# Performance work log

Measured on AMD Instinct MI355X. Metric: run time of the kernel, lower is better.

## Reference

```python
import itertools
import jax, jax.numpy as jnp
import numpy as np

B, S, D = 512, 49, 448
H, KD, RATIO, RES = 8, 32, 4, 7
EKD = KD * RATIO              # expanded key dim = 128
QKV_OUT = H * (2 * KD + EKD)  # 1536
MLP_HID = D * 4               # 1792
EPS = 1e-5
LS_INIT = 1e-5


def _build_bias_idxs():
    points = list(itertools.product(range(RES), range(RES)))
    offsets = {}
    idxs = []
    for p1 in points:
        for p2 in points:
            off = (abs(p1[0] - p2[0]), abs(p1[1] - p2[1]))
            if off not in offsets:
                offsets[off] = len(offsets)
            idxs.append(offsets[off])
    return np.asarray(idxs, dtype=np.int32).reshape(len(points), len(points)), len(offsets)


def setup_inputs() -> dict:
    key = jax.random.key(0)
    ks = jax.random.split(key, 10)
    idxs_np, n_off = _build_bias_idxs()  # (49,49), 49 unique offsets
    std = 0.02
    return {
        "hidden_states": jax.random.normal(ks[0], (B, S, D), jnp.float32),
        "ln1_g": jnp.ones((D,), jnp.float32),
        "ln1_b": jnp.zeros((D,), jnp.float32),
        "qkv_w": jax.random.normal(ks[1], (D, QKV_OUT), jnp.float32) * std,
        "qkv_b": jnp.zeros((QKV_OUT,), jnp.float32),
        "attention_biases": jax.random.normal(ks[2], (H, n_off), jnp.float32) * std,
        "proj_w": jax.random.normal(ks[3], (H * EKD, D), jnp.float32) * std,
        "proj_b": jnp.zeros((D,), jnp.float32),
        "ln2_g": jnp.ones((D,), jnp.float32),
        "ln2_b": jnp.zeros((D,), jnp.float32),
        "mlp_w1": jax.random.normal(ks[4], (D, MLP_HID), jnp.float32) * std,
        "mlp_b1": jnp.zeros((MLP_HID,), jnp.float32),
        "mlp_w2": jax.random.normal(ks[5], (MLP_HID, D), jnp.float32) * std,
        "mlp_b2": jnp.zeros((D,), jnp.float32),
        "ls1": jnp.full((D,), LS_INIT, jnp.float32),
        "ls2": jnp.full((D,), LS_INIT, jnp.float32),
        "attention_bias_idxs": jnp.asarray(idxs_np),
    }


def _layernorm(x, g, b):
    mu = jnp.mean(x, axis=-1, keepdims=True)
    var = jnp.mean(jnp.square(x - mu), axis=-1, keepdims=True)
    return (x - mu) * jax.lax.rsqrt(var + EPS) * g + b


def reference(hidden_states, ln1_g, ln1_b, qkv_w, qkv_b, attention_biases,
              proj_w, proj_b, ln2_g, ln2_b, mlp_w1, mlp_b1, mlp_w2, mlp_b2,
              ls1, ls2, attention_bias_idxs):
    x = hidden_states
    # --- token mixer (self-attention with relative-position bias) ---
    h = _layernorm(x, ln1_g, ln1_b)
    qkv = h @ qkv_w + qkv_b                           # [B,S,1536]
    qkv = qkv.reshape(B, S, H, 2 * KD + EKD)
    q, k, v = jnp.split(qkv, [KD, 2 * KD], axis=3)    # [B,S,H,32/32/128]
    scale = KD ** (-0.5)
    scores = jnp.einsum("bqhd,bkhd->bhqk", q, k) * scale
    bias = attention_biases[:, attention_bias_idxs]   # [H,S,S]
    probs = jax.nn.softmax(scores + bias[None], axis=-1)
    ctx = jnp.einsum("bhqk,bkhd->bqhd", probs, v).reshape(B, S, H * EKD)
    attn_out = ctx @ proj_w + proj_b                  # [B,S,D]
    # --- residual with layerscale (drop_path = identity in eval) ---
    x = x + ls1 * attn_out
    # --- MLP branch ---
    h2 = _layernorm(x, ln2_g, ln2_b)
    m = jax.nn.gelu(h2 @ mlp_w1 + mlp_b1, approximate=False)
    m = m @ mlp_w2 + mlp_b2
    x = x + ls2 * m
    return x
```

## Files before the change

kernel.cpp:

```cpp
#include <hip/hip_runtime.h>
#include <hip/hip_bf16.h>

#define BB 512
#define SS 49
#define DD 448
#define HH 8
#define QKVO 1536
#define MLPH 1792
#define MM (BB*SS)

using bf16_t = __hip_bfloat16;
typedef __attribute__((ext_vector_type(8))) short short8;
typedef __attribute__((ext_vector_type(4))) float f32x4;

__device__ __forceinline__ void gload_lds16(const void* g, void* l) {
  __builtin_amdgcn_global_load_lds(
      (const __attribute__((address_space(1))) void*)g,
      (__attribute__((address_space(3))) void*)l,
      16, 0, 0);
}

__global__ __launch_bounds__(256) void transpose_cast(const float* __restrict__ src,
                                                      bf16_t* __restrict__ dst,
                                                      int R, int C)
{
  __shared__ float tile[32][33];
  const int tx = threadIdx.x & 31, ty = threadIdx.x >> 5;
  const int c0 = blockIdx.x * 32, r0 = blockIdx.y * 32;
#pragma unroll
  for (int i = 0; i < 4; ++i)
    tile[ty + i*8][tx] = src[(size_t)(r0 + ty + i*8) * C + c0 + tx];
  __syncthreads();
#pragma unroll
  for (int i = 0; i < 4; ++i)
    dst[(size_t)(c0 + ty + i*8) * R + r0 + tx] = __float2bfloat16(tile[tx][ty + i*8]);
}

__global__ __launch_bounds__(256) void biasprep_kernel(const float* __restrict__ ab,
                                                       const int* __restrict__ idxs,
                                                       bf16_t* __restrict__ bias_pad)
{
  int idx = blockIdx.x * 256 + threadIdx.x;
  int h = idx >> 12, r = (idx >> 6) & 63, c = idx & 63;
  float v = (r < SS && c < SS) ? ab[h*49 + idxs[r*49 + c]] : -1e30f;
  bias_pad[idx] = __float2bfloat16(v);
}

__global__ __launch_bounds__(256) void ln_kernel(const float* __restrict__ x,
                                                 const float* __restrict__ g,
                                                 const float* __restrict__ b,
                                                 bf16_t* __restrict__ out)
{
  const int w = threadIdx.x >> 6, lane = threadIdx.x & 63;
  const int row = blockIdx.x * 4 + w;
  const float* xr = x + (size_t)row * DD;
  float v[7];
  float s = 0.f;
#pragma unroll
  for (int j = 0; j < 7; ++j) { v[j] = xr[lane + 64*j]; s += v[j]; }
#pragma unroll
  for (int off = 32; off; off >>= 1) s += __shfl_xor(s, off, 64);
  const float mu = s * (1.0f/448.0f);
  float q = 0.f;
#pragma unroll
  for (int j = 0; j < 7; ++j) { float d = v[j] - mu; q += d*d; }
#pragma unroll
  for (int off = 32; off; off >>= 1) q += __shfl_xor(q, off, 64);
  const float rstd = rsqrtf(q * (1.0f/448.0f) + 1e-5f);
  bf16_t* orow = out + (size_t)row * DD;
#pragma unroll
  for (int j = 0; j < 7; ++j) {
    int c = lane + 64*j;
    orow[c] = __float2bfloat16((v[j] - mu) * rstd * g[c] + b[c]);
  }
}

enum { EP_BF16 = 0, EP_RES1 = 1, EP_GELU = 2, EP_RES2 = 3 };

template<int EPI>
__global__ __launch_bounds__(256, 2) void gemmd_bf16(
    const bf16_t* __restrict__ A, const bf16_t* __restrict__ Bt,
    const float* __restrict__ bias, const float* __restrict__ resid,
    const float* __restrict__ ls, bf16_t* __restrict__ Obf,
    float* __restrict__ Of, int N, int K, int gy)
{
  extern __shared__ __align__(16) char lds[];
  const int t = threadIdx.x;
  const int lane = t & 63;
  const int w = t >> 6;

  const int chunk = gridDim.x >> 3;
  const int lin = blockIdx.x;
  const int swz = (lin & 7) * chunk + (lin >> 3);
  const int m0 = (swz / gy) * 128;
  const int n0 = (swz % gy) * 128;

  const int fr = lane & 15;
  const int fq = lane >> 4;
  const int wm = (w >> 1) * 64;
  const int wn = (w & 1) * 64;

  f32x4 acc[4][4];
#pragma unroll
  for (int i = 0; i < 4; ++i)
#pragma unroll
    for (int j = 0; j < 4; ++j)
      acc[i][j] = f32x4{0.f, 0.f, 0.f, 0.f};

  const int rsub = t >> 3;
  const int g8 = (t & 7) ^ (rsub & 7);
  const int wbase = w * 1024;
  const int nkt = K >> 6;

  const bf16_t* gA[4];
  const bf16_t* gB[4];
#pragma unroll
  for (int i = 0; i < 4; ++i) {
    gA[i] = A + (size_t)(m0 + i*32 + rsub) * K + g8*8;
    int rb = n0 + i*32 + rsub;
    if (rb >= N) rb = N - 1;
    gB[i] = Bt + (size_t)rb * K + g8*8;
  }

#pragma unroll
  for (int i = 0; i < 4; ++i) {
    gload_lds16(gA[i], lds + i*4096 + wbase);
    gload_lds16(gB[i], lds + 16384 + i*4096 + wbase);
  }
  __syncthreads();

  int cur = 0;
  for (int kt = 0; kt < nkt; ++kt) {
    if (kt + 1 < nkt) {
      char* db = lds + (cur ^ 1) * 32768;
      const int ko = (kt + 1) << 6;
#pragma unroll
      for (int i = 0; i < 4; ++i) {
        gload_lds16(gA[i] + ko, db + i*4096 + wbase);
        gload_lds16(gB[i] + ko, db + 16384 + i*4096 + wbase);
      }
    }
    const char* sb = lds + cur * 32768;
#pragma unroll
    for (int kk = 0; kk < 2; ++kk) {
      short8 af[4], bfr[4];
#pragma unroll
      for (int i = 0; i < 4; ++i) {
        const int ra = wm + i*16 + fr;
        const int ca = (fq + kk*4) ^ (ra & 7);
        af[i] = *(const short8*)(sb + ra*128 + ca*16);
        const int rb2 = wn + i*16 + fr;
        const int cb = (fq + kk*4) ^ (rb2 & 7);
        bfr[i] = *(const short8*)(sb + 16384 + rb2*128 + cb*16);
      }
#pragma unroll
      for (int mi = 0; mi < 4; ++mi)
#pragma unroll
        for (int ni = 0; ni < 4; ++ni)
          acc[mi][ni] = __builtin_amdgcn_mfma_f32_16x16x32_bf16(af[mi], bfr[ni], acc[mi][ni], 0, 0, 0);
    }
    __syncthreads();
    cur ^= 1;
  }

#pragma unroll
  for (int mi = 0; mi < 4; ++mi) {
#pragma unroll
    for (int ni = 0; ni < 4; ++ni) {
      const int col = n0 + wn + ni*16 + fr;
      if (col < N) {
        const float bc = bias[col];
        const int row0 = m0 + wm + mi*16 + fq*4;
#pragma unroll
        for (int ri = 0; ri < 4; ++ri) {
          const size_t o = (size_t)(row0 + ri) * N + col;
          const float v = acc[mi][ni][ri] + bc;
          if constexpr (EPI == EP_BF16) {
            Obf[o] = __float2bfloat16(v);
          } else if constexpr (EPI == EP_GELU) {
            Obf[o] = __float2bfloat16(0.5f * v * (1.0f + erff(v * 0.7071067811865475f)));
          } else if constexpr (EPI == EP_RES1) {
            Of[o] = resid[o] + ls[col] * v;
          } else {
            Of[o] = Of[o] + ls[col] * v;
          }
        }
      }
    }
  }
}

__global__ __launch_bounds__(64) void attn_mfma_kernel(const bf16_t* __restrict__ qkv,
                                                       const bf16_t* __restrict__ bias_pad,
                                                       bf16_t* __restrict__ ctx)
{
  __shared__ __align__(16) bf16_t VsF[64*128];
  __shared__ __align__(16) bf16_t PsF[64*72];
  const int b = blockIdx.x >> 3, h = blockIdx.x & 7;
  const int l = threadIdx.x;
  const int fr = l & 15, g = l >> 4;
  const size_t base = ((size_t)b * SS) * QKVO + (size_t)h * 192;

  for (int c = l; c < 1024; c += 64) {
    const int j = c >> 4, ch = c & 15;
    const int jc = j < SS ? j : SS - 1;
    short8 v = *(const short8*)(qkv + base + (size_t)jc * QKVO + 64 + ch*8);
    *(short8*)(&VsF[j*128 + ((ch ^ (j >> 3)) & 15)*8]) = v;
  }

  short8 qf[4], kf[4];
#pragma unroll
  for (int mi = 0; mi < 4; ++mi) {
    int qr = mi*16 + fr; if (qr > SS-1) qr = SS-1;
    qf[mi] = *(const short8*)(qkv + base + (size_t)qr * QKVO + g*8);
    int kr = mi*16 + fr; if (kr > SS-1) kr = SS-1;
    kf[mi] = *(const short8*)(qkv + base + (size_t)kr * QKVO + 32 + g*8);
  }
  f32x4 sc[4][4];
#pragma unroll
  for (int mi = 0; mi < 4; ++mi)
#pragma unroll
    for (int ni = 0; ni < 4; ++ni)
      sc[mi][ni] = f32x4{0.f,0.f,0.f,0.f};
#pragma unroll
  for (int mi = 0; mi < 4; ++mi)
#pragma unroll
    for (int ni = 0; ni < 4; ++ni)
      sc[mi][ni] = __builtin_amdgcn_mfma_f32_16x16x32_bf16(qf[mi], kf[ni], sc[mi][ni], 0, 0, 0);

  const float scale = 0.17677669529663687f;
  const bf16_t* bp = bias_pad + (size_t)h * 4096;
#pragma unroll
  for (int mi = 0; mi < 4; ++mi) {
#pragma unroll
    for (int ri = 0; ri < 4; ++ri) {
      const int r = mi*16 + g*4 + ri;
      float v0 = sc[mi][0][ri]*scale + __bfloat162float(bp[r*64 +      fr]);
      float v1 = sc[mi][1][ri]*scale + __bfloat162float(bp[r*64 + 16 + fr]);
      float v2 = sc[mi][2][ri]*scale + __bfloat162float(bp[r*64 + 32 + fr]);
      float v3 = sc[mi][3][ri]*scale + __bfloat162float(bp[r*64 + 48 + fr]);
      float m = fmaxf(fmaxf(v0, v1), fmaxf(v2, v3));
#pragma unroll
      for (int off = 8; off; off >>= 1) m = fmaxf(m, __shfl_xor(m, off, 64));
      v0 = __expf(v0 - m); v1 = __expf(v1 - m);
      v2 = __expf(v2 - m); v3 = __expf(v3 - m);
      float s = v0 + v1 + v2 + v3;
#pragma unroll
      for (int off = 8; off; off >>= 1) s += __shfl_xor(s, off, 64);
      const float inv = 1.0f / s;
      PsF[r*72 +      fr] = __float2bfloat16(v0 * inv);
      PsF[r*72 + 16 + fr] = __float2bfloat16(v1 * inv);
      PsF[r*72 + 32 + fr] = __float2bfloat16(v2 * inv);
      PsF[r*72 + 48 + fr] = __float2bfloat16(v3 * inv);
    }
  }
  __syncthreads();

  short8 pf[4][2];
#pragma unroll
  for (int mi = 0; mi < 4; ++mi)
#pragma unroll
    for (int ks = 0; ks < 2; ++ks)
      pf[mi][ks] = *(const short8*)(&PsF[(mi*16 + fr)*72 + ks*32 + g*8]);

#pragma unroll
  for (int ni = 0; ni < 8; ++ni) {
    const int e = ni*16 + fr;
    short8 vf[2];
#pragma unroll
    for (int ks = 0; ks < 2; ++ks) {
      const int jb = ks*32 + g*8;
#pragma unroll
      for (int jj = 0; jj < 8; ++jj) {
        const int j = jb + jj;
        const int ch = ((e >> 3) ^ (j >> 3)) & 15;
        vf[ks][jj] = *(const short*)(&VsF[j*128 + ch*8 + (e & 7)]);
      }
    }
    f32x4 acc2[4];
#pragma unroll
    for (int mi = 0; mi < 4; ++mi) acc2[mi] = f32x4{0.f,0.f,0.f,0.f};
#pragma unroll
    for (int ks = 0; ks < 2; ++ks)
#pragma unroll
      for (int mi = 0; mi < 4; ++mi)
        acc2[mi] = __builtin_amdgcn_mfma_f32_16x16x32_bf16(pf[mi][ks], vf[ks], acc2[mi], 0, 0, 0);
#pragma unroll
    for (int mi = 0; mi < 4; ++mi) {
#pragma unroll
      for (int ri = 0; ri < 4; ++ri) {
        const int q = mi*16 + g*4 + ri;
        if (q < SS)
          ctx[((size_t)b * SS + q) * 1024 + h*128 + e] = __float2bfloat16(acc2[mi][ri]);
      }
    }
  }
}

extern "C" void kernel_launch(void* const* d_in, const int* in_sizes, int n_in,
                              void* d_out, int out_size, void* d_ws, size_t ws_size,
                              hipStream_t stream) {
  const float* x      = (const float*)d_in[0];
  const float* ln1_g  = (const float*)d_in[1];
  const float* ln1_b  = (const float*)d_in[2];
  const float* qkv_w  = (const float*)d_in[3];
  const float* qkv_b  = (const float*)d_in[4];
  const float* ab     = (const float*)d_in[5];
  const float* proj_w = (const float*)d_in[6];
  const float* proj_b = (const float*)d_in[7];
  const float* ln2_g  = (const float*)d_in[8];
  const float* ln2_b  = (const float*)d_in[9];
  const float* w1     = (const float*)d_in[10];
  const float* b1     = (const float*)d_in[11];
  const float* w2     = (const float*)d_in[12];
  const float* b2     = (const float*)d_in[13];
  const float* ls1    = (const float*)d_in[14];
  const float* ls2    = (const float*)d_in[15];
  const int*   idxs   = (const int*)d_in[16];
  float* out = (float*)d_out;
  char* ws = (char*)d_ws;

  bf16_t* h_buf    = (bf16_t*)(ws);
  bf16_t* qkv_buf  = (bf16_t*)(ws + 22478848);
  bf16_t* ctx_buf  = (bf16_t*)(ws + 99549184);
  bf16_t* m_buf    = (bf16_t*)(ws + 22478848);
  bf16_t* qkv_wT   = (bf16_t*)(ws + 150929408);
  bf16_t* proj_wT  = (bf16_t*)(ws + 152305664);
  bf16_t* w1T      = (bf16_t*)(ws + 153223168);
  bf16_t* w2T      = (bf16_t*)(ws + 154828800);
  bf16_t* bias_pad = (bf16_t*)(ws + 156434432);

  hipFuncSetAttribute((const void*)&gemmd_bf16<EP_BF16>, hipFuncAttributeMaxDynamicSharedMemorySize, 65536);
  hipFuncSetAttribute((const void*)&gemmd_bf16<EP_RES1>, hipFuncAttributeMaxDynamicSharedMemorySize, 65536);
  hipFuncSetAttribute((const void*)&gemmd_bf16<EP_GELU>, hipFuncAttributeMaxDynamicSharedMemorySize, 65536);
  hipFuncSetAttribute((const void*)&gemmd_bf16<EP_RES2>, hipFuncAttributeMaxDynamicSharedMemorySize, 65536);

  transpose_cast<<<dim3(QKVO/32, DD/32),  256, 0, stream>>>(qkv_w,  qkv_wT,  DD,   QKVO);
  transpose_cast<<<dim3(DD/32, 1024/32),  256, 0, stream>>>(proj_w, proj_wT, 1024, DD);
  transpose_cast<<<dim3(MLPH/32, DD/32),  256, 0, stream>>>(w1,     w1T,     DD,   MLPH);
  transpose_cast<<<dim3(DD/32, MLPH/32),  256, 0, stream>>>(w2,     w2T,     MLPH, DD);
  biasprep_kernel<<<128, 256, 0, stream>>>(ab, idxs, bias_pad);

  ln_kernel<<<MM/4, 256, 0, stream>>>(x, ln1_g, ln1_b, h_buf);

  gemmd_bf16<EP_BF16><<<196*12, 256, 65536, stream>>>(
      h_buf, qkv_wT, qkv_b, nullptr, nullptr, qkv_buf, nullptr, QKVO, DD, 12);

  attn_mfma_kernel<<<BB*HH, 64, 0, stream>>>(qkv_buf, bias_pad, ctx_buf);

  gemmd_bf16<EP_RES1><<<196*4, 256, 65536, stream>>>(
      ctx_buf, proj_wT, proj_b, x, ls1, nullptr, out, DD, 1024, 4);

  ln_kernel<<<MM/4, 256, 0, stream>>>(out, ln2_g, ln2_b, h_buf);

  gemmd_bf16<EP_GELU><<<196*14, 256, 65536, stream>>>(
      h_buf, w1T, b1, nullptr, nullptr, m_buf, nullptr, MLPH, DD, 14);

  gemmd_bf16<EP_RES2><<<196*4, 256, 65536, stream>>>(
      m_buf, w2T, b2, nullptr, ls2, nullptr, out, DD, MLPH, 4);
}
```

Before: 385.4 us.

## Split-K narrow-N GEMMs across two warp groups; single-buffer wide GEMMs for occupancy

The wide GEMMs (QKV and MLP up) drop LDS double buffering and use a static 32KB buffer, which allows more resident blocks per CU at the cost of exposing global-load latency behind a barrier. The narrow N=448 GEMMs (proj and MLP down), which have only 784 tiles, now run 512-thread blocks. Each half of the block computes half of K into its own LDS buffer, and the partial sums are reduced through LDS before the residual epilogue. This doubles the waves available per tile on those underfilled launches, but adds an LDS reduction and extra barriers.

```diff
diff --git a/kernel.cpp b/kernel.cpp
--- a/kernel.cpp
+++ b/kernel.cpp
@@ -78,20 +78,19 @@
 enum { EP_BF16 = 0, EP_RES1 = 1, EP_GELU = 2, EP_RES2 = 3 };
 
 template<int EPI>
-__global__ __launch_bounds__(256, 2) void gemmd_bf16(
+__global__ __launch_bounds__(256, 2) void gemmr_bf16(
     const bf16_t* __restrict__ A, const bf16_t* __restrict__ Bt,
     const float* __restrict__ bias, const float* __restrict__ resid,
     const float* __restrict__ ls, bf16_t* __restrict__ Obf,
     float* __restrict__ Of, int N, int K, int gy)
 {
-  extern __shared__ __align__(16) char lds[];
+  __shared__ __align__(16) char lds[32768];
   const int t = threadIdx.x;
   const int lane = t & 63;
   const int w = t >> 6;
 
   const int chunk = gridDim.x >> 3;
-  const int lin = blockIdx.x;
-  const int swz = (lin & 7) * chunk + (lin >> 3);
+  const int swz = (blockIdx.x & 7) * chunk + (blockIdx.x >> 3);
   const int m0 = (swz / gy) * 128;
   const int n0 = (swz % gy) * 128;
 
@@ -122,25 +121,14 @@
     gB[i] = Bt + (size_t)rb * K + g8*8;
   }
 
-#pragma unroll
-  for (int i = 0; i < 4; ++i) {
-    gload_lds16(gA[i], lds + i*4096 + wbase);
-    gload_lds16(gB[i], lds + 16384 + i*4096 + wbase);
-  }
-  __syncthreads();
-
-  int cur = 0;
   for (int kt = 0; kt < nkt; ++kt) {
-    if (kt + 1 < nkt) {
-      char* db = lds + (cur ^ 1) * 32768;
-      const int ko = (kt + 1) << 6;
-#pragma unroll
-      for (int i = 0; i < 4; ++i) {
-        gload_lds16(gA[i] + ko, db + i*4096 + wbase);
-        gload_lds16(gB[i] + ko, db + 16384 + i*4096 + wbase);
-      }
-    }
-    const char* sb = lds + cur * 32768;
+    const int ko = kt << 6;
+#pragma unroll
+    for (int i = 0; i < 4; ++i) {
+      gload_lds16(gA[i] + ko, lds + i*4096 + wbase);
+      gload_lds16(gB[i] + ko, lds + 16384 + i*4096 + wbase);
+    }
+    __syncthreads();
 #pragma unroll
     for (int kk = 0; kk < 2; ++kk) {
       short8 af[4], bfr[4];
@@ -148,10 +136,10 @@
       for (int i = 0; i < 4; ++i) {
         const int ra = wm + i*16 + fr;
         const int ca = (fq + kk*4) ^ (ra & 7);
-        af[i] = *(const short8*)(sb + ra*128 + ca*16);
+        af[i] = *(const short8*)(lds + ra*128 + ca*16);
         const int rb2 = wn + i*16 + fr;
         const int cb = (fq + kk*4) ^ (rb2 & 7);
-        bfr[i] = *(const short8*)(sb + 16384 + rb2*128 + cb*16);
+        bfr[i] = *(const short8*)(lds + 16384 + rb2*128 + cb*16);
       }
 #pragma unroll
       for (int mi = 0; mi < 4; ++mi)
@@ -160,7 +148,6 @@
           acc[mi][ni] = __builtin_amdgcn_mfma_f32_16x16x32_bf16(af[mi], bfr[ni], acc[mi][ni], 0, 0, 0);
     }
     __syncthreads();
-    cur ^= 1;
   }
 
 #pragma unroll
@@ -183,6 +170,125 @@
             Of[o] = resid[o] + ls[col] * v;
           } else {
             Of[o] = Of[o] + ls[col] * v;
+          }
+        }
+      }
+    }
+  }
+}
+
+template<int EPI>
+__global__ __launch_bounds__(512, 4) void gemmsk_bf16(
+    const bf16_t* __restrict__ A, const bf16_t* __restrict__ Bt,
+    const float* __restrict__ bias, const float* __restrict__ resid,
+    const float* __restrict__ ls, bf16_t* __restrict__ Obf,
+    float* __restrict__ Of, int N, int K, int gy)
+{
+  extern __shared__ __align__(16) char lds[];
+  const int t = threadIdx.x;
+  const int lane = t & 63;
+  const int w = t >> 6;
+  const int kg = w >> 2;
+  const int wq = w & 3;
+  const int tg = t & 255;
+  const int Kh = K >> 1;
+
+  const int chunk = gridDim.x >> 3;
+  const int swz = (blockIdx.x & 7) * chunk + (blockIdx.x >> 3);
+  const int m0 = (swz / gy) * 128;
+  const int n0 = (swz % gy) * 128;
+
+  const int fr = lane & 15;
+  const int fq = lane >> 4;
+  const int wm = (wq >> 1) * 64;
+  const int wn = (wq & 1) * 64;
+
+  f32x4 acc[4][4];
+#pragma unroll
+  for (int i = 0; i < 4; ++i)
+#pragma unroll
+    for (int j = 0; j < 4; ++j)
+      acc[i][j] = f32x4{0.f, 0.f, 0.f, 0.f};
+
+  const int rsub = tg >> 3;
+  const int g8 = (tg & 7) ^ (rsub & 7);
+  char* const gbuf = lds + kg * 32768;
+  const int wbase = (tg >> 6) * 1024;
+
+  const bf16_t* gA[4];
+  const bf16_t* gB[4];
+#pragma unroll
+  for (int i = 0; i < 4; ++i) {
+    gA[i] = A + (size_t)(m0 + i*32 + rsub) * K + kg*Kh + g8*8;
+    int rb = n0 + i*32 + rsub;
+    if (rb >= N) rb = N - 1;
+    gB[i] = Bt + (size_t)rb * K + kg*Kh + g8*8;
+  }
+
+  const int nkt = Kh >> 6;
+  for (int kt = 0; kt < nkt; ++kt) {
+    const int ko = kt << 6;
+#pragma unroll
+    for (int i = 0; i < 4; ++i) {
+      gload_lds16(gA[i] + ko, gbuf + i*4096 + wbase);
+      gload_lds16(gB[i] + ko, gbuf + 16384 + i*4096 + wbase);
+    }
+    __syncthreads();
+#pragma unroll
+    for (int kk = 0; kk < 2; ++kk) {
+      short8 af[4], bfr[4];
+#pragma unroll
+      for (int i = 0; i < 4; ++i) {
+        const int ra = wm + i*16 + fr;
+        const int ca = (fq + kk*4) ^ (ra & 7);
+        af[i] = *(const short8*)(gbuf + ra*128 + ca*16);
+        const int rb2 = wn + i*16 + fr;
+        const int cb = (fq + kk*4) ^ (rb2 & 7);
+        bfr[i] = *(const short8*)(gbuf + 16384 + rb2*128 + cb*16);
+      }
+#pragma unroll
+      for (int mi = 0; mi < 4; ++mi)
+#pragma unroll
+        for (int ni = 0; ni < 4; ++ni)
+          acc[mi][ni] = __builtin_amdgcn_mfma_f32_16x16x32_bf16(af[mi], bfr[ni], acc[mi][ni], 0, 0, 0);
+    }
+    __syncthreads();
+  }
+
+  float* red = (float*)lds;
+  if (kg == 1) {
+#pragma unroll
+    for (int mi = 0; mi < 4; ++mi)
+#pragma unroll
+      for (int ni = 0; ni < 4; ++ni) {
+        const int col = wn + ni*16 + fr;
+        const int row0 = wm + mi*16 + fq*4;
+#pragma unroll
+        for (int ri = 0; ri < 4; ++ri)
+          red[(row0 + ri)*128 + col] = acc[mi][ni][ri];
+      }
+  }
+  __syncthreads();
+  if (kg == 0) {
+#pragma unroll
+    for (int mi = 0; mi < 4; ++mi) {
+#pragma unroll
+      for (int ni = 0; ni < 4; ++ni) {
+        const int col = n0 + wn + ni*16 + fr;
+        if (col < N) {
+          const float bc = bias[col];
+          const int row0 = m0 + wm + mi*16 + fq*4;
+          const int lr0 = wm + mi*16 + fq*4;
+          const int lc = wn + ni*16 + fr;
+#pragma unroll
+          for (int ri = 0; ri < 4; ++ri) {
+            const size_t o = (size_t)(row0 + ri) * N + col;
+            const float v = acc[mi][ni][ri] + red[(lr0 + ri)*128 + lc] + bc;
+            if constexpr (EPI == EP_RES1) {
+              Of[o] = resid[o] + ls[col] * v;
+            } else {
+              Of[o] = Of[o] + ls[col] * v;
+            }
           }
         }
       }
@@ -330,10 +436,8 @@
   bf16_t* w2T      = (bf16_t*)(ws + 154828800);
   bf16_t* bias_pad = (bf16_t*)(ws + 156434432);
 
-  hipFuncSetAttribute((const void*)&gemmd_bf16<EP_BF16>, hipFuncAttributeMaxDynamicSharedMemorySize, 65536);
-  hipFuncSetAttribute((const void*)&gemmd_bf16<EP_RES1>, hipFuncAttributeMaxDynamicSharedMemorySize, 65536);
-  hipFuncSetAttribute((const void*)&gemmd_bf16<EP_GELU>, hipFuncAttributeMaxDynamicSharedMemorySize, 65536);
-  hipFuncSetAttribute((const void*)&gemmd_bf16<EP_RES2>, hipFuncAttributeMaxDynamicSharedMemorySize, 65536);
+  hipFuncSetAttribute((const void*)&gemmsk_bf16<EP_RES1>, hipFuncAttributeMaxDynamicSharedMemorySize, 65536);
+  hipFuncSetAttribute((const void*)&gemmsk_bf16<EP_RES2>, hipFuncAttributeMaxDynamicSharedMemorySize, 65536);
 
   transpose_cast<<<dim3(QKVO/32, DD/32),  256, 0, stream>>>(qkv_w,  qkv_wT,  DD,   QKVO);
   transpose_cast<<<dim3(DD/32, 1024/32),  256, 0, stream>>>(proj_w, proj_wT, 1024, DD);
@@ -343,19 +447,19 @@
 
   ln_kernel<<<MM/4, 256, 0, stream>>>(x, ln1_g, ln1_b, h_buf);
 
-  gemmd_bf16<EP_BF16><<<196*12, 256, 65536, stream>>>(
+  gemmr_bf16<EP_BF16><<<196*12, 256, 0, stream>>>(
       h_buf, qkv_wT, qkv_b, nullptr, nullptr, qkv_buf, nullptr, QKVO, DD, 12);
 
   attn_mfma_kernel<<<BB*HH, 64, 0, stream>>>(qkv_buf, bias_pad, ctx_buf);
 
-  gemmd_bf16<EP_RES1><<<196*4, 256, 65536, stream>>>(
+  gemmsk_bf16<EP_RES1><<<196*4, 512, 65536, stream>>>(
       ctx_buf, proj_wT, proj_b, x, ls1, nullptr, out, DD, 1024, 4);
 
   ln_kernel<<<MM/4, 256, 0, stream>>>(out, ln2_g, ln2_b, h_buf);
 
-  gemmd_bf16<EP_GELU><<<196*14, 256, 65536, stream>>>(
+  gemmr_bf16<EP_GELU><<<196*14, 256, 0, stream>>>(
       h_buf, w1T, b1, nullptr, nullptr, m_buf, nullptr, MLPH, DD, 14);
 
-  gemmd_bf16<EP_RES2><<<196*4, 256, 65536, stream>>>(
+  gemmsk_bf16<EP_RES2><<<196*4, 512, 65536, stream>>>(
       m_buf, w2T, b2, nullptr, ls2, nullptr, out, DD, MLPH, 4);
 }
```

New measurement: 354.6 us. 8.0% less time.
